# Performance work log

Hardware: AMD Instinct MI355X
Metric: run time of the kernel (lower is better)

The kernel has to match this reference:

```python
import jax, jax.numpy as jnp
import numpy as np

ACT_DIM = 768
DICT_SIZE = 16384
K = 64
BATCH = 2048


def setup_inputs() -> dict:
    key = jax.random.key(0)
    k_x, k_w, k_be = jax.random.split(key, 3)
    x = jax.random.normal(k_x, (BATCH, ACT_DIM), dtype=jnp.float32)
    # encoder weight [dict_size, act_dim]; decoder initialized as encoder.T with unit-norm columns
    W_enc = jax.random.normal(k_w, (DICT_SIZE, ACT_DIM), dtype=jnp.float32) * 0.02
    b_enc = jnp.zeros((DICT_SIZE,), dtype=jnp.float32)
    W_dec = W_enc.T  # [act_dim, dict_size]
    eps = jnp.finfo(jnp.float32).eps
    W_dec = W_dec / (jnp.linalg.norm(W_dec, axis=0, keepdims=True) + eps)
    b_dec = jnp.zeros((ACT_DIM,), dtype=jnp.float32)
    return {"x": x, "W_enc": W_enc, "b_enc": b_enc, "W_dec": W_dec, "b_dec": b_dec}


def reference(x, W_enc, b_enc, W_dec, b_dec):
    B = x.shape[0]
    # encode: linear on (x - b_dec), relu
    post_relu_BF = jax.nn.relu((x - b_dec) @ W_enc.T + b_enc)  # [B, F]
    flat = post_relu_BF.reshape(-1)  # [B*F]
    # global batch top-k: keep k*B largest activations across the whole batch
    vals, idx = jax.lax.top_k(flat, K * B)
    encoded_flat = jnp.zeros_like(flat).at[idx].set(vals)
    encoded_BF = encoded_flat.reshape(post_relu_BF.shape)
    # decode
    x_hat_BD = encoded_BF @ W_dec.T + b_dec  # [B, D]
    return x_hat_BD
```

## Files before the change

### kernel.cpp

```cpp
#include <hip/hip_runtime.h>
#include <stdint.h>

#define BATCH   2048
#define DIM     768
#define FEAT    16384
#define KSEL    64
#define KB_SEL  (BATCH * KSEL)
#define N_TOT   (BATCH * FEAT)
#define NX4     (BATCH * DIM / 4)
#define NW4     (FEAT * DIM / 4)

#define GBM 128
#define GBN 128
#define GBK 32
#define AROW   24
#define APLANE 3088

#define MARGIN  32768
#define CCAP    229376
#define TIE_CAP 1024
#define LSTAGE  2048
#define FG      8
#define FBLK    (CCAP / (FG * 4))

#define SL_T32    0
#define SL_NC     1
#define SL_DEF    2
#define SL_NTIE   3
#define SL_WIN    4
#define SL_S0     16

typedef __attribute__((ext_vector_type(8))) __bf16 bf16x8;
typedef __attribute__((ext_vector_type(4))) float  f32x4;
typedef unsigned long long u64;

__device__ __forceinline__ unsigned short bf16r(float v)
{
    unsigned u = __float_as_uint(v);
    u += 0x7FFFu + ((u >> 16) & 1u);
    return (unsigned short)(u >> 16);
}

__device__ __forceinline__ unsigned wave_append(unsigned* counter, bool pred)
{
    unsigned long long m = __ballot(pred);
    if (m == 0ull) return 0xFFFFFFFFu;
    const int lane = threadIdx.x & 63;
    const int leader = __ffsll((unsigned long long)m) - 1;
    unsigned base = 0;
    if (lane == leader) base = atomicAdd(counter, (unsigned)__popcll(m));
    base = __shfl(base, leader, 64);
    if (!pred) return 0xFFFFFFFFu;
    return base + (unsigned)__popcll(m & ((1ull << lane) - 1ull));
}

__global__ __launch_bounds__(256) void sae16_prep(const float* __restrict__ x,
                                                  const float* __restrict__ Wenc,
                                                  const float* __restrict__ bdec,
                                                  unsigned short* __restrict__ xb,
                                                  unsigned short* __restrict__ wb)
{
    const int tot = NX4 + NW4;
    for (int i = blockIdx.x * 256 + threadIdx.x; i < tot; i += gridDim.x * 256) {
        if (i < NX4) {
            const int e = i * 4;
            const int d = e % DIM;
            float4 v  = *(const float4*)(x + e);
            float4 dv = *(const float4*)(bdec + d);
            uint2 p;
            p.x = (unsigned)bf16r(v.x - dv.x) | ((unsigned)bf16r(v.y - dv.y) << 16);
            p.y = (unsigned)bf16r(v.z - dv.z) | ((unsigned)bf16r(v.w - dv.w) << 16);
            *(uint2*)(xb + e) = p;
        } else {
            const int e = (i - NX4) * 4;
            float4 v = *(const float4*)(Wenc + e);
            uint2 p;
            p.x = (unsigned)bf16r(v.x) | ((unsigned)bf16r(v.y) << 16);
            p.y = (unsigned)bf16r(v.z) | ((unsigned)bf16r(v.w) << 16);
            *(uint2*)(wb + e) = p;
        }
    }
}

__global__ __launch_bounds__(256) void sae16_gemm(const unsigned short* __restrict__ xb,
                                                  const unsigned short* __restrict__ wb,
                                                  const float* __restrict__ benc,
                                                  unsigned short* __restrict__ Yb)
{
    __shared__ unsigned short Als[4 * APLANE];
    __shared__ unsigned short Bls[4 * APLANE];

    const int tid  = threadIdx.x;
    const int row0 = blockIdx.y * GBM;
    const int col0 = blockIdx.x * GBN;
    const int wid  = tid >> 6;
    const int lane = tid & 63;
    const int wr = wid >> 1;
    const int wc = wid & 1;
    const int fr = lane & 15;
    const int kg = lane >> 4;

    f32x4 acc[4][4];
#pragma unroll
    for (int i = 0; i < 4; ++i)
#pragma unroll
        for (int j = 0; j < 4; ++j) acc[i][j] = (f32x4){0.f, 0.f, 0.f, 0.f};

    for (int kt = 0; kt < DIM; kt += GBK) {
#pragma unroll
        for (int i = 0; i < 4; ++i) {
            const int idx = i * 256 + tid;
            const int r   = idx >> 3;
            const int kq  = (idx & 7) * 4;
            const int g   = kq >> 3;
            const int k0  = kq & 7;
            *(uint2*)&Als[g * APLANE + r * AROW + k0] =
                *(const uint2*)(xb + (size_t)(row0 + r) * DIM + kt + kq);
            *(uint2*)&Bls[g * APLANE + r * AROW + k0] =
                *(const uint2*)(wb + (size_t)(col0 + r) * DIM + kt + kq);
        }
        __syncthreads();

        bf16x8 afr[4], bfr[4];
#pragma unroll
        for (int mi = 0; mi < 4; ++mi)
            afr[mi] = *(const bf16x8*)&Als[kg * APLANE + (wr * 64 + mi * 16 + fr) * AROW];
#pragma unroll
        for (int ni = 0; ni < 4; ++ni)
            bfr[ni] = *(const bf16x8*)&Bls[kg * APLANE + (wc * 64 + ni * 16 + fr) * AROW];
#pragma unroll
        for (int mi = 0; mi < 4; ++mi)
#pragma unroll
            for (int ni = 0; ni < 4; ++ni)
                acc[mi][ni] = __builtin_amdgcn_mfma_f32_16x16x32_bf16(
                    afr[mi], bfr[ni], acc[mi][ni], 0, 0, 0);
        __syncthreads();
    }

#pragma unroll
    for (int ni = 0; ni < 4; ++ni) {
        const int col = col0 + wc * 64 + ni * 16 + fr;
        const float be = benc[col];
#pragma unroll
        for (int mi = 0; mi < 4; ++mi) {
            const int rbase = row0 + wr * 64 + mi * 16 + kg * 4;
#pragma unroll
            for (int j = 0; j < 4; ++j)
                Yb[(size_t)(rbase + j) * FEAT + col] =
                    bf16r(fmaxf(acc[mi][ni][j] + be, 0.f));
        }
    }
}

__global__ void sae16_wt(const float* __restrict__ Wdec, float* __restrict__ Wt)
{
    __shared__ float t[32][33];
    const int f0 = blockIdx.x * 32;
    const int d0 = blockIdx.y * 32;
    const int tx = threadIdx.x;
    const int ty = threadIdx.y;
#pragma unroll
    for (int i = 0; i < 4; ++i)
        t[ty + i * 8][tx] = Wdec[(size_t)(d0 + ty + i * 8) * FEAT + f0 + tx];
    __syncthreads();
#pragma unroll
    for (int i = 0; i < 4; ++i)
        Wt[(size_t)(f0 + ty + i * 8) * DIM + d0 + tx] = t[tx][ty + i * 8];
}

__global__ __launch_bounds__(1024) void sae16_hist(const unsigned short* __restrict__ Yb,
                                                   unsigned* __restrict__ hist)
{
    __shared__ unsigned h[16384];
    const int t = threadIdx.x;
    for (int i = t; i < 16384; i += 1024) h[i] = 0u;
    __syncthreads();
    const uint4* Y8 = (const uint4*)Yb;
    const int total8 = N_TOT / 8;
    for (int i = blockIdx.x * 1024 + t; i < total8; i += gridDim.x * 1024) {
        uint4 v = Y8[i];
        unsigned w[4] = {v.x, v.y, v.z, v.w};
#pragma unroll
        for (int k = 0; k < 4; ++k) {
            unsigned lo = w[k] & 0xFFFFu;
            unsigned hi = w[k] >> 16;
            if (lo) atomicAdd(&h[lo >> 2], 1u);
            if (hi) atomicAdd(&h[hi >> 2], 1u);
        }
    }
    __syncthreads();
    for (int i = t; i < 16384; i += 1024) {
        unsigned c = h[i];
        if (c) atomicAdd(&hist[i], c);
    }
}

__global__ __launch_bounds__(1024) void sae16_selb(const unsigned* __restrict__ hist,
                                                   unsigned* sl)
{
    __shared__ unsigned s[1024];
    const int t = threadIdx.x;
    const int C = 16;
    const unsigned N = (unsigned)(KB_SEL + MARGIN);
    const int lo = t * C;
    unsigned S = 0;
    for (int i = 0; i < C; ++i) S += hist[lo + i];
    s[t] = S;
    __syncthreads();
    for (int off = 1; off < 1024; off <<= 1) {
        unsigned v = (t + off < 1024) ? s[t + off] : 0u;
        __syncthreads();
        s[t] += v;
        __syncthreads();
    }
    const unsigned incl  = s[t];
    const unsigned above = incl - S;
    if (above < N && N <= incl) {
        unsigned cum = above;
        for (int i = lo + C - 1; i >= lo; --i) {
            cum += hist[i];
            if (cum >= N) { sl[SL_T32] = (unsigned)i << 2; break; }
        }
    }
}

__global__ __launch_bounds__(256) void sae16_cand(const unsigned short* __restrict__ Yb,
                                                  unsigned* __restrict__ sl,
                                                  int* __restrict__ cand_raw)
{
    __shared__ int      loc[LSTAGE];
    __shared__ unsigned lcnt;
    __shared__ unsigned gbase;
    if (threadIdx.x == 0) lcnt = 0;
    __syncthreads();

    const unsigned T = sl[SL_T32];
    const uint4* Y8 = (const uint4*)Yb;
    const int total8 = N_TOT / 8;
    for (int i = blockIdx.x * blockDim.x + threadIdx.x; i < total8;
         i += gridDim.x * blockDim.x) {
        uint4 v = Y8[i];
        unsigned w[4] = {v.x, v.y, v.z, v.w};
#pragma unroll
        for (int k = 0; k < 4; ++k) {
            unsigned lo = w[k] & 0xFFFFu;
            unsigned hi = w[k] >> 16;
            if (lo >= T) {
                unsigned p = atomicAdd(&lcnt, 1u);
                if (p < (unsigned)LSTAGE) loc[p] = i * 8 + k * 2;
            }
            if (hi >= T) {
                unsigned p = atomicAdd(&lcnt, 1u);
                if (p < (unsigned)LSTAGE) loc[p] = i * 8 + k * 2 + 1;
            }
        }
    }
    __syncthreads();
    unsigned n = lcnt;
    if (n > (unsigned)LSTAGE) n = (unsigned)LSTAGE;
    if (threadIdx.x == 0) gbase = atomicAdd(&sl[SL_NC], n);
    __syncthreads();
    const unsigned base = gbase;
    for (unsigned k = threadIdx.x; k < n; k += blockDim.x) {
        unsigned dst = base + k;
        if (dst < (unsigned)CCAP) cand_raw[dst] = loc[k];
    }
}

__global__ __launch_bounds__(256) void sae16_fhist(const int* __restrict__ cand_raw,
                                                   const unsigned* __restrict__ sl,
                                                   unsigned* __restrict__ fhist)
{
    __shared__ unsigned h[16384];
    const int t = threadIdx.x;
    for (int i = t; i < 16384; i += 256) h[i] = 0u;
    __syncthreads();
    unsigned NC = sl[SL_NC];
    if (NC > (unsigned)CCAP) NC = (unsigned)CCAP;
    for (int i = blockIdx.x * 256 + t; i < (int)NC; i += gridDim.x * 256)
        atomicAdd(&h[cand_raw[i] & (FEAT - 1)], 1u);
    __syncthreads();
    for (int i = t; i < 16384; i += 256) {
        unsigned c = h[i];
        if (c) atomicAdd(&fhist[i], c);
    }
}

__global__ __launch_bounds__(1024) void sae16_fscan(const unsigned* __restrict__ fhist,
                                                    unsigned* __restrict__ fofs)
{
    __shared__ unsigned s[1024];
    const int t = threadIdx.x;
    unsigned c[16];
    unsigned sum = 0;
#pragma unroll
    for (int j = 0; j < 16; ++j) { c[j] = fhist[t * 16 + j]; sum += c[j]; }
    s[t] = sum;
    __syncthreads();
    for (int off = 1; off < 1024; off <<= 1) {
        unsigned v = (t >= off) ? s[t - off] : 0u;
        __syncthreads();
        s[t] += v;
        __syncthreads();
    }
    unsigned run = s[t] - sum;
#pragma unroll
    for (int j = 0; j < 16; ++j) { fofs[t * 16 + j] = run; run += c[j]; }
}

__global__ __launch_bounds__(256) void sae16_fscat(const int* __restrict__ cand_raw,
                                                   const unsigned* __restrict__ sl,
                                                   const unsigned* __restrict__ fofs,
                                                   unsigned* __restrict__ fcur,
                                                   int* __restrict__ cand_flat)
{
    unsigned NC = sl[SL_NC];
    if (NC > (unsigned)CCAP) NC = (unsigned)CCAP;
    for (int i = blockIdx.x * 256 + threadIdx.x; i < (int)NC; i += gridDim.x * 256) {
        int flat = cand_raw[i];
        int f = flat & (FEAT - 1);
        unsigned p = atomicAdd(&fcur[f], 1u);
        unsigned dst = fofs[f] + p;
        if (dst < (unsigned)CCAP) cand_flat[dst] = flat;
    }
}

__global__ __launch_bounds__(256) void sae16_feval(const float* __restrict__ x,
                                                   const float* __restrict__ Wenc,
                                                   const float* __restrict__ benc,
                                                   const float* __restrict__ bdec,
                                                   const unsigned* __restrict__ sl,
                                                   const int* __restrict__ cand_flat,
                                                   u64* __restrict__ cand_key)
{
    unsigned NC = sl[SL_NC];
    if (NC > (unsigned)CCAP) NC = (unsigned)CCAP;
    const int lane = threadIdx.x & 63;
    const int b = blockIdx.x;
    const int lb = (b & 7) * (FBLK / 8) + (b >> 3);
    const int wid = lb * 4 + (threadIdx.x >> 6);
    const int c0 = wid * FG;
    if (c0 >= (int)NC) return;

    float bd[12], wv[12];
#pragma unroll
    for (int j = 0; j < 12; ++j) bd[j] = bdec[lane + j * 64];
    int fprev = -1;

    for (int g = 0; g < FG; ++g) {
        const int c = c0 + g;
        if (c >= (int)NC) break;
        const int flat = cand_flat[c];
        const int bb = flat >> 14;
        const int f  = flat & (FEAT - 1);
        if (f != fprev) {
            const float* wr = Wenc + (size_t)f * DIM;
#pragma unroll
            for (int j = 0; j < 12; ++j) wv[j] = wr[lane + j * 64];
            fprev = f;
        }
        const float* xr = x + (size_t)bb * DIM;
        double p = 0.0;
#pragma unroll
        for (int j = 0; j < 12; ++j)
            p = fma((double)xr[lane + j * 64] - (double)bd[j], (double)wv[j], p);
#pragma unroll
        for (int o = 32; o > 0; o >>= 1) p += __shfl_xor(p, o, 64);
        if (lane == 0) {
            p += (double)benc[f];
            if (p < 0.0) p = 0.0;
            cand_key[c] = (u64)__double_as_longlong(p);
        }
    }
}

__global__ __launch_bounds__(256) void sae16_hist64(const u64* __restrict__ cand_key,
                                                    const unsigned* __restrict__ sl,
                                                    unsigned* __restrict__ hist,
                                                    int pass)
{
    __shared__ unsigned h[16384];
    const int t = threadIdx.x;
    for (int i = t; i < 16384; i += 256) h[i] = 0u;
    __syncthreads();

    unsigned NC = sl[SL_NC];
    if (NC > (unsigned)CCAP) NC = (unsigned)CCAP;
    u64 pref = 0;
    for (int i = 0; i < pass; ++i) pref = (pref << 14) | (u64)sl[SL_S0 + i];
    const int chk_sh = 64 - 14 * pass;
    const int bkt_sh = 50 - 14 * pass;

    for (int i = blockIdx.x * 256 + t; i < (int)NC; i += gridDim.x * 256) {
        u64 key = cand_key[i];
        if (pass > 0 && (key >> chk_sh) != pref) continue;
        atomicAdd(&h[(unsigned)(key >> bkt_sh) & 0x3FFFu], 1u);
    }
    __syncthreads();
    for (int i = t; i < 16384; i += 256) {
        unsigned c = h[i];
        if (c) atomicAdd(&hist[i], c);
    }
}

__global__ __launch_bounds__(1024) void sae16_sel14(const unsigned* __restrict__ hist,
                                                    unsigned* sl, int pass)
{
    __shared__ unsigned s[1024];
    const int t = threadIdx.x;
    const int C = 16;
    const unsigned N = (pass == 0) ? (unsigned)KB_SEL : sl[SL_S0 + 4 + pass - 1];
    const int lo = t * C;
    unsigned S = 0;
    for (int i = 0; i < C; ++i) S += hist[lo + i];
    s[t] = S;
    __syncthreads();
    for (int off = 1; off < 1024; off <<= 1) {
        unsigned v = (t + off < 1024) ? s[t + off] : 0u;
        __syncthreads();
        s[t] += v;
        __syncthreads();
    }
    const unsigned incl  = s[t];
    const unsigned above = incl - S;
    if (above < N && N <= incl) {
        unsigned cum = above;
        for (int i = lo + C - 1; i >= lo; --i) {
            cum += hist[i];
            if (cum >= N) {
                sl[SL_S0 + pass]     = (unsigned)i;
                sl[SL_S0 + 4 + pass] = N - (cum - hist[i]);
                break;
            }
        }
    }
}

__global__ __launch_bounds__(256) void sae16_maxb(const u64* __restrict__ cand_key,
                                                  const unsigned* __restrict__ sl,
                                                  u64* __restrict__ mx)
{
    unsigned NC = sl[SL_NC];
    if (NC > (unsigned)CCAP) NC = (unsigned)CCAP;
    const u64 Tsh1 = ((u64)sl[SL_S0 + 0] << 28) | ((u64)sl[SL_S0 + 1] << 14) |
                     (u64)sl[SL_S0 + 2];
    u64 m = 0;
    for (int i = blockIdx.x * 256 + threadIdx.x; i < (int)NC; i += gridDim.x * 256) {
        u64 k = cand_key[i];
        if ((k >> 22) < Tsh1 && k > m) m = k;
    }
#pragma unroll
    for (int o = 32; o > 0; o >>= 1) {
        u64 o2 = __shfl_xor(m, o, 64);
        if (o2 > m) m = o2;
    }
    if ((threadIdx.x & 63) == 0 && m) atomicMax((unsigned long long*)mx, m);
}

__global__ __launch_bounds__(256) void sae16_class(const u64* __restrict__ cand_key,
                                                   const int* __restrict__ cand_flat,
                                                   const u64* __restrict__ mx,
                                                   unsigned* __restrict__ sl,
                                                   unsigned* __restrict__ row_cnt,
                                                   int* __restrict__ sel_flat,
                                                   float* __restrict__ sel_val,
                                                   int* __restrict__ tie_flat,
                                                   u64* __restrict__ tie_key)
{
    unsigned NC = sl[SL_NC];
    if (NC > (unsigned)CCAP) NC = (unsigned)CCAP;
    const u64 Tsh1 = ((u64)sl[SL_S0 + 0] << 28) | ((u64)sl[SL_S0 + 1] << 14) |
                     (u64)sl[SL_S0 + 2];
    const u64 Tsh2 = mx[0] >> 22;
    const int c = blockIdx.x * 256 + threadIdx.x;
    const bool active = (c < (int)NC);
    u64 key = 0;
    int flat = 0;
    u64 keysh = 0;
    if (active) {
        key = cand_key[c];
        keysh = key >> 22;
        flat = cand_flat[c];
    }
    const bool selp = active && (keysh > Tsh1);
    unsigned p = wave_append(&sl[SL_DEF], selp);
    if (selp && p < (unsigned)KB_SEL) {
        sel_flat[p] = flat;
        sel_val[p]  = (float)__longlong_as_double((long long)key);
        atomicAdd(&row_cnt[flat >> 14], 1u);
    }
    const bool tiep = active && !selp && (keysh == Tsh2);
    unsigned q = wave_append(&sl[SL_NTIE], tiep);
    if (tiep && q < (unsigned)TIE_CAP) { tie_flat[q] = flat; tie_key[q] = key; }
}

__global__ __launch_bounds__(256) void sae16_ties(const int* __restrict__ tie_flat,
                                                  const u64* __restrict__ tie_key,
                                                  unsigned* __restrict__ sl,
                                                  int* __restrict__ sel_flat,
                                                  float* __restrict__ sel_val,
                                                  unsigned* __restrict__ row_cnt)
{
    unsigned R = sl[SL_NTIE];
    if (R > (unsigned)TIE_CAP) R = (unsigned)TIE_CAP;
    const unsigned REM = sl[SL_S0 + 6];
    const unsigned D = sl[SL_DEF];
    const int c = blockIdx.x * blockDim.x + threadIdx.x;
    if (c >= (int)R) return;
    const int ic = tie_flat[c];
    unsigned rank = 0;
    for (int j = 0; j < (int)R; ++j)
        if (tie_flat[j] < ic) ++rank;
    if (rank < REM) {
        unsigned p = D + atomicAdd(&sl[SL_WIN], 1u);
        if (p < (unsigned)KB_SEL) {
            sel_flat[p] = ic;
            sel_val[p]  = (float)__longlong_as_double((long long)tie_key[c]);
            atomicAdd(&row_cnt[ic >> 14], 1u);
        }
    }
}

__global__ __launch_bounds__(256) void sae16_scan(const unsigned* __restrict__ row_cnt,
                                                  unsigned* __restrict__ row_ofs)
{
    __shared__ unsigned s[256];
    const int t = threadIdx.x;
    unsigned c[8];
    unsigned sum = 0;
#pragma unroll
    for (int j = 0; j < 8; ++j) { c[j] = row_cnt[t * 8 + j]; sum += c[j]; }
    s[t] = sum;
    __syncthreads();
    for (int off = 1; off < 256; off <<= 1) {
        unsigned v = (t >= off) ? s[t - off] : 0u;
        __syncthreads();
        s[t] += v;
        __syncthreads();
    }
    unsigned run = s[t] - sum;
#pragma unroll
    for (int j = 0; j < 8; ++j) { row_ofs[t * 8 + j] = run; run += c[j]; }
    if (t == 255) row_ofs[2048] = run;
}

__global__ void sae16_scatter(const int* __restrict__ sel_flat,
                              const float* __restrict__ sel_val,
                              const unsigned* __restrict__ row_ofs,
                              unsigned* __restrict__ cursor,
                              int* __restrict__ gf, float* __restrict__ gv)
{
    int e = blockIdx.x * blockDim.x + threadIdx.x;
    if (e >= KB_SEL) return;
    int flat = sel_flat[e];
    int b = flat >> 14;
    unsigned p = atomicAdd(&cursor[b], 1u);
    unsigned dst = row_ofs[b] + p;
    if (dst < (unsigned)KB_SEL) {
        gf[dst] = flat & (FEAT - 1);
        gv[dst] = sel_val[e];
    }
}

__global__ __launch_bounds__(256) void sae16_decode(const int* __restrict__ gf,
                                                    const float* __restrict__ gv,
                                                    const unsigned* __restrict__ row_ofs,
                                                    const float* __restrict__ Wt,
                                                    const float* __restrict__ bdec,
                                                    float* __restrict__ out)
{
    const int b = blockIdx.x;
    const int t = threadIdx.x;
    float a0 = 0.f, a1 = 0.f, a2 = 0.f;
    const unsigned s = row_ofs[b];
    const unsigned e = row_ofs[b + 1];
    for (unsigned i = s; i < e; ++i) {
        const int f   = gf[i];
        const float v = gv[i];
        const float* w = Wt + (size_t)f * DIM;
        a0 = fmaf(v, w[t], a0);
        a1 = fmaf(v, w[t + 256], a1);
        a2 = fmaf(v, w[t + 512], a2);
    }
    out[(size_t)b * DIM + t]       = a0 + bdec[t];
    out[(size_t)b * DIM + t + 256] = a1 + bdec[t + 256];
    out[(size_t)b * DIM + t + 512] = a2 + bdec[t + 512];
}

extern "C" void kernel_launch(void* const* d_in, const int* in_sizes, int n_in,
                              void* d_out, int out_size, void* d_ws, size_t ws_size,
                              hipStream_t stream)
{
    (void)in_sizes; (void)n_in; (void)out_size;
    const float* x    = (const float*)d_in[0];
    const float* Wenc = (const float*)d_in[1];
    const float* benc = (const float*)d_in[2];
    const float* Wdec = (const float*)d_in[3];
    const float* bdec = (const float*)d_in[4];
    float* out = (float*)d_out;

    char* ws = (char*)d_ws;
    size_t off = 0;
    unsigned short* Yb  = (unsigned short*)(ws + off);     off += (size_t)N_TOT * 2;
    float*    Wt        = (float*)(ws + off);              off += (size_t)FEAT * DIM * 4;
    unsigned short* xb  = (unsigned short*)(ws + off);     off += (size_t)BATCH * DIM * 2;
    unsigned short* wb  = (unsigned short*)(ws + off);     off += (size_t)FEAT * DIM * 2;
    u64*      cand_key  = (u64*)(ws + off);                off += (size_t)CCAP * 8;
    int*      cand_raw  = (int*)(ws + off);                off += (size_t)CCAP * 4;
    int*      cand_flat = (int*)(ws + off);                off += (size_t)CCAP * 4;
    int*      tie_flat  = (int*)(ws + off);                off += (size_t)TIE_CAP * 4;
    u64*      tie_key   = (u64*)(ws + off);                off += (size_t)TIE_CAP * 8;
    unsigned* row_ofs   = (unsigned*)(ws + off);           off += 2052 * 4;
    unsigned* fofs      = (unsigned*)(ws + off);           off += 16384 * 4;
    char* zstart = ws + off;
    int*      sel_flat  = (int*)(ws + off);                off += (size_t)KB_SEL * 4;
    float*    sel_val   = (float*)(ws + off);              off += (size_t)KB_SEL * 4;
    int*      gf        = (int*)(ws + off);                off += (size_t)KB_SEL * 4;
    float*    gv        = (float*)(ws + off);              off += (size_t)KB_SEL * 4;
    unsigned* hist1     = (unsigned*)(ws + off);           off += 16384 * 4;
    unsigned* h64       = (unsigned*)(ws + off);           off += 3 * 16384 * 4;
    unsigned* fhist     = (unsigned*)(ws + off);           off += 16384 * 4;
    unsigned* fcur      = (unsigned*)(ws + off);           off += 16384 * 4;
    unsigned* row_cnt   = (unsigned*)(ws + off);           off += 2048 * 4;
    unsigned* cursor    = (unsigned*)(ws + off);           off += 2048 * 4;
    u64*      mx        = (u64*)(ws + off);                off += 8;
    unsigned* sl        = (unsigned*)(ws + off);           off += 256;
    const size_t zbytes = (size_t)((ws + off) - zstart);
    if (ws_size < off) return;

    hipMemsetAsync(zstart, 0, zbytes, stream);

    sae16_prep<<<4096, 256, 0, stream>>>(x, Wenc, bdec, xb, wb);
    sae16_wt<<<dim3(FEAT / 32, DIM / 32), dim3(32, 8), 0, stream>>>(Wdec, Wt);
    sae16_gemm<<<dim3(FEAT / GBN, BATCH / GBM), 256, 0, stream>>>(xb, wb, benc, Yb);

    sae16_hist<<<512, 1024, 0, stream>>>(Yb, hist1);
    sae16_selb<<<1, 1024, 0, stream>>>(hist1, sl);

    sae16_cand<<<2048, 256, 0, stream>>>(Yb, sl, cand_raw);
    sae16_fhist<<<256, 256, 0, stream>>>(cand_raw, sl, fhist);
    sae16_fscan<<<1, 1024, 0, stream>>>(fhist, fofs);
    sae16_fscat<<<256, 256, 0, stream>>>(cand_raw, sl, fofs, fcur, cand_flat);
    sae16_feval<<<FBLK, 256, 0, stream>>>(x, Wenc, benc, bdec, sl, cand_flat, cand_key);

    for (int p = 0; p < 3; ++p) {
        sae16_hist64<<<256, 256, 0, stream>>>(cand_key, sl, h64 + p * 16384, p);
        sae16_sel14<<<1, 1024, 0, stream>>>(h64 + p * 16384, sl, p);
    }
    sae16_maxb<<<256, 256, 0, stream>>>(cand_key, sl, mx);

    sae16_class<<<(CCAP + 255) / 256, 256, 0, stream>>>(cand_key, cand_flat, mx, sl, row_cnt,
                                                        sel_flat, sel_val, tie_flat, tie_key);
    sae16_ties<<<TIE_CAP / 256, 256, 0, stream>>>(tie_flat, tie_key, sl,
                                                  sel_flat, sel_val, row_cnt);

    sae16_scan<<<1, 256, 0, stream>>>(row_cnt, row_ofs);
    sae16_scatter<<<(KB_SEL + 255) / 256, 256, 0, stream>>>(sel_flat, sel_val, row_ofs, cursor, gf, gv);
    sae16_decode<<<BATCH, 256, 0, stream>>>(gf, gv, row_ofs, Wt, bdec, out);
}
```

Before: 462.8 us.

## Estimate top-k threshold from strided sample and store decoder weights in bf16

The full-pass histogram over the whole bf16 activation matrix is replaced by a 1-in-64 strided sample, with 8192 bins. The candidate threshold is picked so that about 3072 sampled values lie above it. Candidate capacity grows to absorb the larger statistical spread, and exact top-k refinement still follows. Separately, the transposed decoder weights are written and gathered as bf16 instead of fp32, halving transpose writes and decode gather traffic. The risks are candidate overflow or too few candidates when the sample is unrepresentative, and extra rounding error in the decode.

Result: faster. 449.1 us (-3.0%).

```diff
diff --git a/kernel.cpp b/kernel.cpp
--- a/kernel.cpp
+++ b/kernel.cpp
@@ -16,8 +16,8 @@
 #define AROW   24
 #define APLANE 3088
 
-#define MARGIN  32768
-#define CCAP    229376
+#define SAMP_N  3072
+#define CCAP    262144
 #define TIE_CAP 1024
 #define LSTAGE  2048
 #define FG      8
@@ -54,7 +54,7 @@
     return base + (unsigned)__popcll(m & ((1ull << lane) - 1ull));
 }
 
-__global__ __launch_bounds__(256) void sae16_prep(const float* __restrict__ x,
+__global__ __launch_bounds__(256) void sae17_prep(const float* __restrict__ x,
                                                   const float* __restrict__ Wenc,
                                                   const float* __restrict__ bdec,
                                                   unsigned short* __restrict__ xb,
@@ -82,7 +82,7 @@
     }
 }
 
-__global__ __launch_bounds__(256) void sae16_gemm(const unsigned short* __restrict__ xb,
+__global__ __launch_bounds__(256) void sae17_gemm(const unsigned short* __restrict__ xb,
                                                   const unsigned short* __restrict__ wb,
                                                   const float* __restrict__ benc,
                                                   unsigned short* __restrict__ Yb)
@@ -152,7 +152,8 @@
     }
 }
 
-__global__ void sae16_wt(const float* __restrict__ Wdec, float* __restrict__ Wt)
+__global__ void sae17_wt(const float* __restrict__ Wdec,
+                         unsigned short* __restrict__ Wtb)
 {
     __shared__ float t[32][33];
     const int f0 = blockIdx.x * 32;
@@ -165,19 +166,20 @@
     __syncthreads();
 #pragma unroll
     for (int i = 0; i < 4; ++i)
-        Wt[(size_t)(f0 + ty + i * 8) * DIM + d0 + tx] = t[tx][ty + i * 8];
-}
-
-__global__ __launch_bounds__(1024) void sae16_hist(const unsigned short* __restrict__ Yb,
+        Wtb[(size_t)(f0 + ty + i * 8) * DIM + d0 + tx] = bf16r(t[tx][ty + i * 8]);
+}
+
+__global__ __launch_bounds__(256) void sae17_shist(const unsigned short* __restrict__ Yb,
                                                    unsigned* __restrict__ hist)
 {
-    __shared__ unsigned h[16384];
-    const int t = threadIdx.x;
-    for (int i = t; i < 16384; i += 1024) h[i] = 0u;
+    __shared__ unsigned h[8192];
+    const int t = threadIdx.x;
+    for (int i = t; i < 8192; i += 256) h[i] = 0u;
     __syncthreads();
     const uint4* Y8 = (const uint4*)Yb;
-    const int total8 = N_TOT / 8;
-    for (int i = blockIdx.x * 1024 + t; i < total8; i += gridDim.x * 1024) {
+    const int idx = blockIdx.x * 256 + t;
+    const int i = idx * 64;
+    if (i < N_TOT / 8) {
         uint4 v = Y8[i];
         unsigned w[4] = {v.x, v.y, v.z, v.w};
 #pragma unroll
@@ -189,19 +191,19 @@
         }
     }
     __syncthreads();
-    for (int i = t; i < 16384; i += 1024) {
-        unsigned c = h[i];
-        if (c) atomicAdd(&hist[i], c);
-    }
-}
-
-__global__ __launch_bounds__(1024) void sae16_selb(const unsigned* __restrict__ hist,
+    for (int i2 = t; i2 < 8192; i2 += 256) {
+        unsigned c = h[i2];
+        if (c) atomicAdd(&hist[i2], c);
+    }
+}
+
+__global__ __launch_bounds__(1024) void sae17_selb(const unsigned* __restrict__ hist,
                                                    unsigned* sl)
 {
     __shared__ unsigned s[1024];
     const int t = threadIdx.x;
-    const int C = 16;
-    const unsigned N = (unsigned)(KB_SEL + MARGIN);
+    const int C = 8;
+    const unsigned N = (unsigned)SAMP_N;
     const int lo = t * C;
     unsigned S = 0;
     for (int i = 0; i < C; ++i) S += hist[lo + i];
@@ -224,7 +226,7 @@
     }
 }
 
-__global__ __launch_bounds__(256) void sae16_cand(const unsigned short* __restrict__ Yb,
+__global__ __launch_bounds__(256) void sae17_cand(const unsigned short* __restrict__ Yb,
                                                   unsigned* __restrict__ sl,
                                                   int* __restrict__ cand_raw)
 {
@@ -267,7 +269,7 @@
     }
 }
 
-__global__ __launch_bounds__(256) void sae16_fhist(const int* __restrict__ cand_raw,
+__global__ __launch_bounds__(256) void sae17_fhist(const int* __restrict__ cand_raw,
                                                    const unsigned* __restrict__ sl,
                                                    unsigned* __restrict__ fhist)
 {
@@ -286,7 +288,7 @@
     }
 }
 
-__global__ __launch_bounds__(1024) void sae16_fscan(const unsigned* __restrict__ fhist,
+__global__ __launch_bounds__(1024) void sae17_fscan(const unsigned* __restrict__ fhist,
                                                     unsigned* __restrict__ fofs)
 {
     __shared__ unsigned s[1024];
@@ -308,7 +310,7 @@
     for (int j = 0; j < 16; ++j) { fofs[t * 16 + j] = run; run += c[j]; }
 }
 
-__global__ __launch_bounds__(256) void sae16_fscat(const int* __restrict__ cand_raw,
+__global__ __launch_bounds__(256) void sae17_fscat(const int* __restrict__ cand_raw,
                                                    const unsigned* __restrict__ sl,
                                                    const unsigned* __restrict__ fofs,
                                                    unsigned* __restrict__ fcur,
@@ -325,7 +327,7 @@
     }
 }
 
-__global__ __launch_bounds__(256) void sae16_feval(const float* __restrict__ x,
+__global__ __launch_bounds__(256) void sae17_feval(const float* __restrict__ x,
                                                    const float* __restrict__ Wenc,
                                                    const float* __restrict__ benc,
                                                    const float* __restrict__ bdec,
@@ -374,7 +376,7 @@
     }
 }
 
-__global__ __launch_bounds__(256) void sae16_hist64(const u64* __restrict__ cand_key,
+__global__ __launch_bounds__(256) void sae17_hist64(const u64* __restrict__ cand_key,
                                                     const unsigned* __restrict__ sl,
                                                     unsigned* __restrict__ hist,
                                                     int pass)
@@ -403,7 +405,7 @@
     }
 }
 
-__global__ __launch_bounds__(1024) void sae16_sel14(const unsigned* __restrict__ hist,
+__global__ __launch_bounds__(1024) void sae17_sel14(const unsigned* __restrict__ hist,
                                                     unsigned* sl, int pass)
 {
     __shared__ unsigned s[1024];
@@ -436,7 +438,7 @@
     }
 }
 
-__global__ __launch_bounds__(256) void sae16_maxb(const u64* __restrict__ cand_key,
+__global__ __launch_bounds__(256) void sae17_maxb(const u64* __restrict__ cand_key,
                                                   const unsigned* __restrict__ sl,
                                                   u64* __restrict__ mx)
 {
@@ -457,7 +459,7 @@
     if ((threadIdx.x & 63) == 0 && m) atomicMax((unsigned long long*)mx, m);
 }
 
-__global__ __launch_bounds__(256) void sae16_class(const u64* __restrict__ cand_key,
+__global__ __launch_bounds__(256) void sae17_class(const u64* __restrict__ cand_key,
                                                    const int* __restrict__ cand_flat,
                                                    const u64* __restrict__ mx,
                                                    unsigned* __restrict__ sl,
@@ -494,7 +496,7 @@
     if (tiep && q < (unsigned)TIE_CAP) { tie_flat[q] = flat; tie_key[q] = key; }
 }
 
-__global__ __launch_bounds__(256) void sae16_ties(const int* __restrict__ tie_flat,
+__global__ __launch_bounds__(256) void sae17_ties(const int* __restrict__ tie_flat,
                                                   const u64* __restrict__ tie_key,
                                                   unsigned* __restrict__ sl,
                                                   int* __restrict__ sel_flat,
@@ -521,7 +523,7 @@
     }
 }
 
-__global__ __launch_bounds__(256) void sae16_scan(const unsigned* __restrict__ row_cnt,
+__global__ __launch_bounds__(256) void sae17_scan(const unsigned* __restrict__ row_cnt,
                                                   unsigned* __restrict__ row_ofs)
 {
     __shared__ unsigned s[256];
@@ -544,7 +546,7 @@
     if (t == 255) row_ofs[2048] = run;
 }
 
-__global__ void sae16_scatter(const int* __restrict__ sel_flat,
+__global__ void sae17_scatter(const int* __restrict__ sel_flat,
                               const float* __restrict__ sel_val,
                               const unsigned* __restrict__ row_ofs,
                               unsigned* __restrict__ cursor,
@@ -562,10 +564,10 @@
     }
 }
 
-__global__ __launch_bounds__(256) void sae16_decode(const int* __restrict__ gf,
+__global__ __launch_bounds__(256) void sae17_decode(const int* __restrict__ gf,
                                                     const float* __restrict__ gv,
                                                     const unsigned* __restrict__ row_ofs,
-                                                    const float* __restrict__ Wt,
+                                                    const unsigned short* __restrict__ Wtb,
                                                     const float* __restrict__ bdec,
                                                     float* __restrict__ out)
 {
@@ -577,10 +579,10 @@
     for (unsigned i = s; i < e; ++i) {
         const int f   = gf[i];
         const float v = gv[i];
-        const float* w = Wt + (size_t)f * DIM;
-        a0 = fmaf(v, w[t], a0);
-        a1 = fmaf(v, w[t + 256], a1);
-        a2 = fmaf(v, w[t + 512], a2);
+        const unsigned short* w = Wtb + (size_t)f * DIM;
+        a0 = fmaf(v, __uint_as_float((unsigned)w[t]       << 16), a0);
+        a1 = fmaf(v, __uint_as_float((unsigned)w[t + 256] << 16), a1);
+        a2 = fmaf(v, __uint_as_float((unsigned)w[t + 512] << 16), a2);
     }
     out[(size_t)b * DIM + t]       = a0 + bdec[t];
     out[(size_t)b * DIM + t + 256] = a1 + bdec[t + 256];
@@ -602,7 +604,7 @@
     char* ws = (char*)d_ws;
     size_t off = 0;
     unsigned short* Yb  = (unsigned short*)(ws + off);     off += (size_t)N_TOT * 2;
-    float*    Wt        = (float*)(ws + off);              off += (size_t)FEAT * DIM * 4;
+    unsigned short* Wtb = (unsigned short*)(ws + off);     off += (size_t)FEAT * DIM * 2;
     unsigned short* xb  = (unsigned short*)(ws + off);     off += (size_t)BATCH * DIM * 2;
     unsigned short* wb  = (unsigned short*)(ws + off);     off += (size_t)FEAT * DIM * 2;
     u64*      cand_key  = (u64*)(ws + off);                off += (size_t)CCAP * 8;
@@ -617,7 +619,7 @@
     float*    sel_val   = (float*)(ws + off);              off += (size_t)KB_SEL * 4;
     int*      gf        = (int*)(ws + off);                off += (size_t)KB_SEL * 4;
     float*    gv        = (float*)(ws + off);              off += (size_t)KB_SEL * 4;
-    unsigned* hist1     = (unsigned*)(ws + off);           off += 16384 * 4;
+    unsigned* hist1     = (unsigned*)(ws + off);           off += 8192 * 4;
     unsigned* h64       = (unsigned*)(ws + off);           off += 3 * 16384 * 4;
     unsigned* fhist     = (unsigned*)(ws + off);           off += 16384 * 4;
     unsigned* fcur      = (unsigned*)(ws + off);           off += 16384 * 4;
@@ -630,31 +632,31 @@
 
     hipMemsetAsync(zstart, 0, zbytes, stream);
 
-    sae16_prep<<<4096, 256, 0, stream>>>(x, Wenc, bdec, xb, wb);
-    sae16_wt<<<dim3(FEAT / 32, DIM / 32), dim3(32, 8), 0, stream>>>(Wdec, Wt);
-    sae16_gemm<<<dim3(FEAT / GBN, BATCH / GBM), 256, 0, stream>>>(xb, wb, benc, Yb);
-
-    sae16_hist<<<512, 1024, 0, stream>>>(Yb, hist1);
-    sae16_selb<<<1, 1024, 0, stream>>>(hist1, sl);
-
-    sae16_cand<<<2048, 256, 0, stream>>>(Yb, sl, cand_raw);
-    sae16_fhist<<<256, 256, 0, stream>>>(cand_raw, sl, fhist);
-    sae16_fscan<<<1, 1024, 0, stream>>>(fhist, fofs);
-    sae16_fscat<<<256, 256, 0, stream>>>(cand_raw, sl, fofs, fcur, cand_flat);
-    sae16_feval<<<FBLK, 256, 0, stream>>>(x, Wenc, benc, bdec, sl, cand_flat, cand_key);
+    sae17_prep<<<4096, 256, 0, stream>>>(x, Wenc, bdec, xb, wb);
+    sae17_wt<<<dim3(FEAT / 32, DIM / 32), dim3(32, 8), 0, stream>>>(Wdec, Wtb);
+    sae17_gemm<<<dim3(FEAT / GBN, BATCH / GBM), 256, 0, stream>>>(xb, wb, benc, Yb);
+
+    sae17_shist<<<256, 256, 0, stream>>>(Yb, hist1);
+    sae17_selb<<<1, 1024, 0, stream>>>(hist1, sl);
+
+    sae17_cand<<<2048, 256, 0, stream>>>(Yb, sl, cand_raw);
+    sae17_fhist<<<256, 256, 0, stream>>>(cand_raw, sl, fhist);
+    sae17_fscan<<<1, 1024, 0, stream>>>(fhist, fofs);
+    sae17_fscat<<<256, 256, 0, stream>>>(cand_raw, sl, fofs, fcur, cand_flat);
+    sae17_feval<<<FBLK, 256, 0, stream>>>(x, Wenc, benc, bdec, sl, cand_flat, cand_key);
 
     for (int p = 0; p < 3; ++p) {
-        sae16_hist64<<<256, 256, 0, stream>>>(cand_key, sl, h64 + p * 16384, p);
-        sae16_sel14<<<1, 1024, 0, stream>>>(h64 + p * 16384, sl, p);
-    }
-    sae16_maxb<<<256, 256, 0, stream>>>(cand_key, sl, mx);
-
-    sae16_class<<<(CCAP + 255) / 256, 256, 0, stream>>>(cand_key, cand_flat, mx, sl, row_cnt,
+        sae17_hist64<<<256, 256, 0, stream>>>(cand_key, sl, h64 + p * 16384, p);
+        sae17_sel14<<<1, 1024, 0, stream>>>(h64 + p * 16384, sl, p);
+    }
+    sae17_maxb<<<256, 256, 0, stream>>>(cand_key, sl, mx);
+
+    sae17_class<<<(CCAP + 255) / 256, 256, 0, stream>>>(cand_key, cand_flat, mx, sl, row_cnt,
                                                         sel_flat, sel_val, tie_flat, tie_key);
-    sae16_ties<<<TIE_CAP / 256, 256, 0, stream>>>(tie_flat, tie_key, sl,
+    sae17_ties<<<TIE_CAP / 256, 256, 0, stream>>>(tie_flat, tie_key, sl,
                                                   sel_flat, sel_val, row_cnt);
 
-    sae16_scan<<<1, 256, 0, stream>>>(row_cnt, row_ofs);
-    sae16_scatter<<<(KB_SEL + 255) / 256, 256, 0, stream>>>(sel_flat, sel_val, row_ofs, cursor, gf, gv);
-    sae16_decode<<<BATCH, 256, 0, stream>>>(gf, gv, row_ofs, Wt, bdec, out);
-}
+    sae17_scan<<<1, 256, 0, stream>>>(row_cnt, row_ofs);
+    sae17_scatter<<<(KB_SEL + 255) / 256, 256, 0, stream>>>(sel_flat, sel_val, row_ofs, cursor, gf, gv);
+    sae17_decode<<<BATCH, 256, 0, stream>>>(gf, gv, row_ofs, Wtb, bdec, out);
+}
```
